# Performance work log

Hardware: AMD Instinct MI355X
Metric: run time of the kernel (lower is better)

## Reference

```python
import jax, jax.numpy as jnp
import numpy as np

NUM_FEATURES = 256   # 2**8
BOND_DIM = 16
N_CORES = 8          # log2(NUM_FEATURES)
BATCH = 262144


def _mpo_cores(mpo_weights, n, bond_dim):
    # Slice the flat parameter vector into n cores of shape (l, r, 2, 2).
    shapes = [(1, bond_dim, 2, 2)] + [(bond_dim, bond_dim, 2, 2)] * (n - 2) + [(bond_dim, 1, 2, 2)]
    cores, off = [], 0
    for s in shapes:
        sz = int(np.prod(s))
        cores.append(mpo_weights[off:off + sz].reshape(s))
        off += sz
    return cores


def _contract_mpo(cores):
    # Sequentially contract the tensor-train cores into the full (2^n, 2^n) matrix.
    # T has axes (bond, I, J) where I/J accumulate the row/col physical bits
    # in order i1..in / j1..jn, matching the original einsum + reshape.
    T = cores[0][0]          # (r, 2, 2)
    dim = 2
    for A in cores[1:]:      # A: (l, r2, 2, 2)
        T = jnp.einsum('aIJ,abkm->bIkJm', T, A).reshape(A.shape[1], dim * 2, dim * 2)
        dim *= 2
    return T[0]              # (2^n, 2^n)


def setup_inputs() -> dict:
    key = jax.random.key(0)
    k1, k2, k3 = jax.random.split(key, 3)
    total = 2 * 4 * BOND_DIM + (N_CORES - 2) * 4 * BOND_DIM ** 2  # 6272
    return {
        'x': jax.random.normal(k1, (BATCH, NUM_FEATURES), dtype=jnp.float32),
        'mpo_weights': jax.random.normal(k2, (total,), dtype=jnp.float32) * 0.1,
        'dense_kernel': jax.random.normal(k3, (NUM_FEATURES, 1), dtype=jnp.float32) * 0.1,
        'dense_bias': jnp.zeros((1,), dtype=jnp.float32),
    }


def reference(x, mpo_weights, dense_kernel, dense_bias):
    W = _contract_mpo(_mpo_cores(mpo_weights, N_CORES, BOND_DIM))  # (256, 256)
    h = jnp.square(x @ W)                                          # (B, 256)
    return h @ dense_kernel + dense_bias                           # (B, 1)
```

## Files before the change

kernel.cpp:

```cpp
#include <hip/hip_runtime.h>
#include <hip/hip_bf16.h>

typedef _Float16 half8 __attribute__((ext_vector_type(8)));
typedef float    floatx4 __attribute__((ext_vector_type(4)));

#define WSCALE      4096.0f
#define WSCALE_INV  (1.0f/(4096.0f*4096.0f))

#define T1_OFF   0
#define U_OFF    4096
#define WF16_OFF 8192

__global__ __launch_bounds__(1024)
void mpo_prep1(const float* __restrict__ w, float* __restrict__ ws) {
    __shared__ float wL[3136];
    __shared__ float sL[4352];
    const int tid = threadIdx.x;

    if (blockIdx.x == 0) {
        for (int i = tid; i < 3136; i += 1024) wL[i] = w[i];
        __syncthreads();
        if (tid < 256) {
            int li = tid;
            int mm = li & 3, kk = (li >> 2) & 3, c = li >> 4;
            int k1 = kk >> 1, k2 = kk & 1, m1 = mm >> 1, m2 = mm & 1;
            float s = 0.f;
            for (int b = 0; b < 16; ++b)
                s += wL[(b * 2 + k1) * 2 + m1] * wL[64 + ((b * 16 + c) * 2 + k2) * 2 + m2];
            sL[li] = s;
        }
        for (int li = tid; li < 4096; li += 1024) {
            int mm = li & 3, kk = (li >> 2) & 3, ac = li >> 4;
            int c = ac & 15, a = ac >> 4;
            int k1 = kk >> 1, k2 = kk & 1, m1 = mm >> 1, m2 = mm & 1;
            float s = 0.f;
            for (int b = 0; b < 16; ++b)
                s += wL[1088 + ((a * 16 + b) * 2 + k1) * 2 + m1]
                   * wL[2112 + ((b * 16 + c) * 2 + k2) * 2 + m2];
            sL[256 + li] = s;
        }
        __syncthreads();
        for (int idx = tid; idx < 4096; idx += 1024) {
            int J4 = idx & 15; int t = idx >> 4; int I4 = t & 15; int b = t >> 4;
            int I = I4 >> 2, k = I4 & 3, J = J4 >> 2, m = J4 & 3;
            float s = 0.f;
            for (int a = 0; a < 16; ++a)
                s += sL[a * 16 + I * 4 + J] * sL[256 + ((a * 16 + b) * 4 + k) * 4 + m];
            ws[T1_OFF + idx] = s;
        }
    } else {
        for (int i = tid; i < 3136; i += 1024) wL[i] = w[3136 + i];
        __syncthreads();
        for (int li = tid; li < 4096; li += 1024) {
            int mm = li & 3, kk = (li >> 2) & 3, ac = li >> 4;
            int c = ac & 15, a = ac >> 4;
            int k1 = kk >> 1, k2 = kk & 1, m1 = mm >> 1, m2 = mm & 1;
            float s = 0.f;
            for (int b = 0; b < 16; ++b)
                s += wL[((a * 16 + b) * 2 + k1) * 2 + m1]
                   * wL[1024 + ((b * 16 + c) * 2 + k2) * 2 + m2];
            sL[li] = s;
        }
        if (tid < 256) {
            int li = tid;
            int mm = li & 3, kk = (li >> 2) & 3, a = li >> 4;
            int k1 = kk >> 1, k2 = kk & 1, m1 = mm >> 1, m2 = mm & 1;
            float s = 0.f;
            for (int b = 0; b < 16; ++b)
                s += wL[2048 + ((a * 16 + b) * 2 + k1) * 2 + m1]
                   * wL[3072 + (b * 2 + k2) * 2 + m2];
            sL[4096 + li] = s;
        }
        __syncthreads();
        for (int idx = tid; idx < 4096; idx += 1024) {
            int m2 = idx & 3, k2 = (idx >> 2) & 3, mc = (idx >> 4) & 3,
                kc = (idx >> 6) & 3, a = idx >> 8;
            float s = 0.f;
            for (int b = 0; b < 16; ++b)
                s += sL[((a * 16 + b) * 4 + kc) * 4 + mc] * sL[4096 + (b * 4 + k2) * 4 + m2];
            ws[U_OFF + idx] = s;
        }
    }
}

__global__ __launch_bounds__(256)
void mpo_prep2(const float* __restrict__ ws, _Float16* __restrict__ Wf) {
    int idx = blockIdx.x * blockDim.x + threadIdx.x;
    int J4 = idx & 255, I4 = idx >> 8;
    int I16 = I4 >> 4, kc = (I4 >> 2) & 3, k2 = I4 & 3;
    int J16 = J4 >> 4, mc = (J4 >> 2) & 3, m2 = J4 & 3;
    const float* T1 = ws + T1_OFF;
    const float* U  = ws + U_OFF + (((kc * 4 + mc) * 4 + k2) * 4 + m2);
    float s = 0.f;
#pragma unroll
    for (int a = 0; a < 16; ++a)
        s += T1[(a * 16 + I16) * 16 + J16] * U[a * 256];
    int n = J4 >> 4, lr = J4 & 15, kk = I4 >> 5, gg = (I4 >> 3) & 3, j = I4 & 7;
    Wf[(((n * 8 + kk) * 64) + gg * 16 + lr) * 8 + j] = (_Float16)(s * WSCALE);
}

__global__ __launch_bounds__(512, 2)
void mpo_main(const float* __restrict__ x, const _Float16* __restrict__ Wf,
              const float* __restrict__ dk, const float* __restrict__ bias,
              float* __restrict__ out) {
    extern __shared__ _Float16 Wl[];
    float* dkL = reinterpret_cast<float*>(Wl + 65536);

    const int tid  = threadIdx.x;
    const int lane = tid & 63;
    const int wave = tid >> 6;
    const int lrow = lane & 15;
    const int g    = lane >> 4;

    const long blockbase = (long)blockIdx.x * 1024;
    const float* xb0 = x + (blockbase + wave * 16 + lrow) * 256 + g * 8;

    half8 a[8];
    floatx4 lo[8], hi[8];

#define SB()    __builtin_amdgcn_sched_barrier(0)
#define XLD(i, xn) do { const float* p_ = (xn) + (i) * 32;                                  \
                     lo[i] = __builtin_nontemporal_load(reinterpret_cast<const floatx4*>(p_));     \
                     hi[i] = __builtin_nontemporal_load(reinterpret_cast<const floatx4*>(p_ + 4)); \
                   } while (0)
#define XLD_ALL(xn) do { XLD(0,xn); XLD(1,xn); XLD(2,xn); XLD(3,xn);           \
                         XLD(4,xn); XLD(5,xn); XLD(6,xn); XLD(7,xn); } while (0)
#define XCVT(i) do { half8 f_;                                                 \
                     f_[0] = (_Float16)lo[i][0]; f_[1] = (_Float16)lo[i][1];   \
                     f_[2] = (_Float16)lo[i][2]; f_[3] = (_Float16)lo[i][3];   \
                     f_[4] = (_Float16)hi[i][0]; f_[5] = (_Float16)hi[i][1];   \
                     f_[6] = (_Float16)hi[i][2]; f_[7] = (_Float16)hi[i][3];   \
                     a[i] = f_; } while (0)
#define XCVT_ALL() do { XCVT(0); XCVT(1); XCVT(2); XCVT(3);                    \
                        XCVT(4); XCVT(5); XCVT(6); XCVT(7); } while (0)

    XLD_ALL(xb0);
    SB();
    {
        const floatx4* src = reinterpret_cast<const floatx4*>(Wf);
        floatx4* dst = reinterpret_cast<floatx4*>(Wl);
#pragma unroll
        for (int i = 0; i < 16; ++i)
            dst[tid + i * 512] = src[tid + i * 512];
    }
    if (tid < 256) dkL[tid] = dk[tid];
    const float bs = bias[0];
    __syncthreads();

    XCVT_ALL();
    SB();

    const half8* Wv = reinterpret_cast<const half8*>(Wl);

#pragma unroll 1
    for (int p = 0; p < 8; ++p) {
        if (p < 7) {
            const float* xn = xb0 + (p + 1) * (128 * 256);
            XLD_ALL(xn);
        }
        SB();

        float rp[4] = {0, 0, 0, 0};
#pragma unroll 1
        for (int n = 0; n < 16; ++n) {
            const float kv = dkL[n * 16 + lrow];
            const half8* Wn = Wv + n * 512 + lane;
            floatx4 c0 = {0, 0, 0, 0};
#pragma unroll
            for (int kk = 0; kk < 8; ++kk)
                c0 = __builtin_amdgcn_mfma_f32_16x16x32_f16(a[kk], Wn[kk * 64], c0, 0, 0, 0);
#pragma unroll
            for (int r = 0; r < 4; ++r)
                rp[r] += c0[r] * c0[r] * kv;
        }

        if (p < 7) { XCVT_ALL(); }
        SB();

#pragma unroll
        for (int r = 0; r < 4; ++r) {
            float v = rp[r];
            v += __shfl_xor(v, 1);
            v += __shfl_xor(v, 2);
            v += __shfl_xor(v, 4);
            v += __shfl_xor(v, 8);
            rp[r] = v;
        }
        if (lrow == 0) {
            floatx4 o;
#pragma unroll
            for (int r = 0; r < 4; ++r) o[r] = rp[r] * WSCALE_INV + bs;
            *reinterpret_cast<floatx4*>(out + blockbase + p * 128 + wave * 16 + g * 4) = o;
        }
    }
}

extern "C" void kernel_launch(void* const* d_in, const int* in_sizes, int n_in,
                              void* d_out, int out_size, void* d_ws, size_t ws_size,
                              hipStream_t stream) {
    const float* x    = (const float*)d_in[0];
    const float* w    = (const float*)d_in[1];
    const float* dk   = (const float*)d_in[2];
    const float* bias = (const float*)d_in[3];
    float* out = (float*)d_out;
    float* ws  = (float*)d_ws;

    _Float16* Wf16 = (_Float16*)(ws + WF16_OFF);

    static bool attr_set = false;
    if (!attr_set) {
        hipFuncSetAttribute((const void*)mpo_main,
                            hipFuncAttributeMaxDynamicSharedMemorySize, 132096);
        attr_set = true;
    }

    mpo_prep1<<<2, 1024, 0, stream>>>(w, ws);
    mpo_prep2<<<256, 256, 0, stream>>>(ws, Wf16);

    mpo_main<<<256, 512, 132096, stream>>>(x, Wf16, dk, bias, out);
}
```

Baseline: 70.41 us.

## Double-buffer x prefetch two tiles ahead and register-tile MPO prep contractions

The main kernel now keeps two register buffers for x (even/odd tiles), so each tile's loads are issued two iterations ahead and have a full MFMA pass to arrive before conversion. The prep kernel is rewritten to use 256 threads, each computing a 4x4 register tile with vectorized shared-memory reads and a vectorized weight load. Together these aim to hide global load latency in the main loop and shorten the serial prep stage. The extra 32 float4 registers for the second x buffer raise register pressure under the 2-blocks-per-CU launch bound and could cause spilling.

```diff
diff --git a/kernel.cpp b/kernel.cpp
--- a/kernel.cpp
+++ b/kernel.cpp
@@ -11,74 +11,127 @@
 #define U_OFF    4096
 #define WF16_OFF 8192
 
-__global__ __launch_bounds__(1024)
+__global__ __launch_bounds__(256)
 void mpo_prep1(const float* __restrict__ w, float* __restrict__ ws) {
-    __shared__ float wL[3136];
-    __shared__ float sL[4352];
+    __shared__ __align__(16) float wL[3136];
+    __shared__ __align__(16) float sL[4352];
     const int tid = threadIdx.x;
 
+    {
+        const floatx4* s4 = reinterpret_cast<const floatx4*>(w + blockIdx.x * 3136);
+        floatx4* d4 = reinterpret_cast<floatx4*>(wL);
+        for (int i = tid; i < 784; i += 256) d4[i] = s4[i];
+    }
+    __syncthreads();
+
     if (blockIdx.x == 0) {
-        for (int i = tid; i < 3136; i += 1024) wL[i] = w[i];
-        __syncthreads();
-        if (tid < 256) {
+        {
             int li = tid;
             int mm = li & 3, kk = (li >> 2) & 3, c = li >> 4;
             int k1 = kk >> 1, k2 = kk & 1, m1 = mm >> 1, m2 = mm & 1;
             float s = 0.f;
+#pragma unroll
             for (int b = 0; b < 16; ++b)
-                s += wL[(b * 2 + k1) * 2 + m1] * wL[64 + ((b * 16 + c) * 2 + k2) * 2 + m2];
+                s += wL[b * 4 + k1 * 2 + m1] * wL[64 + b * 64 + c * 4 + k2 * 2 + m2];
             sL[li] = s;
         }
-        for (int li = tid; li < 4096; li += 1024) {
-            int mm = li & 3, kk = (li >> 2) & 3, ac = li >> 4;
-            int c = ac & 15, a = ac >> 4;
-            int k1 = kk >> 1, k2 = kk & 1, m1 = mm >> 1, m2 = mm & 1;
-            float s = 0.f;
-            for (int b = 0; b < 16; ++b)
-                s += wL[1088 + ((a * 16 + b) * 2 + k1) * 2 + m1]
-                   * wL[2112 + ((b * 16 + c) * 2 + k2) * 2 + m2];
-            sL[256 + li] = s;
+        {
+            const int i0 = (tid >> 4) * 4, j0 = (tid & 15) * 4;
+            const float* Ab = wL + 1088 + (i0 >> 2) * 64;
+            const float* Bb = wL + 2112 + j0;
+            float acc[4][4] = {};
+#pragma unroll
+            for (int b = 0; b < 16; ++b) {
+                floatx4 ar = *reinterpret_cast<const floatx4*>(Ab + b * 4);
+                floatx4 br = *reinterpret_cast<const floatx4*>(Bb + b * 64);
+#pragma unroll
+                for (int r = 0; r < 4; ++r)
+#pragma unroll
+                    for (int s = 0; s < 4; ++s) acc[r][s] += ar[r] * br[s];
+            }
+#pragma unroll
+            for (int r = 0; r < 4; ++r)
+#pragma unroll
+            for (int s = 0; s < 4; ++s) {
+                int i = i0 + r, j = j0 + s;
+                sL[256 + (i >> 2) * 256 + (j >> 2) * 16 +
+                   ((i >> 1) & 1) * 8 + ((j >> 1) & 1) * 4 + (i & 1) * 2 + (j & 1)] = acc[r][s];
+            }
         }
         __syncthreads();
-        for (int idx = tid; idx < 4096; idx += 1024) {
-            int J4 = idx & 15; int t = idx >> 4; int I4 = t & 15; int b = t >> 4;
-            int I = I4 >> 2, k = I4 & 3, J = J4 >> 2, m = J4 & 3;
-            float s = 0.f;
-            for (int a = 0; a < 16; ++a)
-                s += sL[a * 16 + I * 4 + J] * sL[256 + ((a * 16 + b) * 4 + k) * 4 + m];
-            ws[T1_OFF + idx] = s;
+        {
+            const int p0 = (tid >> 6) * 4, q0 = (tid & 63) * 4;
+            float acc[4][4] = {};
+#pragma unroll
+            for (int a = 0; a < 16; ++a) {
+                floatx4 pr = *reinterpret_cast<const floatx4*>(sL + a * 16 + p0);
+                floatx4 qr = *reinterpret_cast<const floatx4*>(sL + 256 + a * 256 + q0);
+#pragma unroll
+                for (int r = 0; r < 4; ++r)
+#pragma unroll
+                    for (int s = 0; s < 4; ++s) acc[r][s] += pr[r] * qr[s];
+            }
+#pragma unroll
+            for (int r = 0; r < 4; ++r)
+#pragma unroll
+            for (int s = 0; s < 4; ++s) {
+                int p = p0 + r, q = q0 + s;
+                ws[T1_OFF + (q >> 4) * 256 + ((p >> 2) * 4 + ((q >> 2) & 3)) * 16 +
+                   (p & 3) * 4 + (q & 3)] = acc[r][s];
+            }
         }
     } else {
-        for (int i = tid; i < 3136; i += 1024) wL[i] = w[3136 + i];
-        __syncthreads();
-        for (int li = tid; li < 4096; li += 1024) {
-            int mm = li & 3, kk = (li >> 2) & 3, ac = li >> 4;
-            int c = ac & 15, a = ac >> 4;
-            int k1 = kk >> 1, k2 = kk & 1, m1 = mm >> 1, m2 = mm & 1;
-            float s = 0.f;
-            for (int b = 0; b < 16; ++b)
-                s += wL[((a * 16 + b) * 2 + k1) * 2 + m1]
-                   * wL[1024 + ((b * 16 + c) * 2 + k2) * 2 + m2];
-            sL[li] = s;
-        }
-        if (tid < 256) {
+        {
+            const int i0 = (tid >> 4) * 4, j0 = (tid & 15) * 4;
+            const float* Ab = wL + (i0 >> 2) * 64;
+            const float* Bb = wL + 1024 + j0;
+            float acc[4][4] = {};
+#pragma unroll
+            for (int b = 0; b < 16; ++b) {
+                floatx4 ar = *reinterpret_cast<const floatx4*>(Ab + b * 4);
+                floatx4 br = *reinterpret_cast<const floatx4*>(Bb + b * 64);
+#pragma unroll
+                for (int r = 0; r < 4; ++r)
+#pragma unroll
+                    for (int s = 0; s < 4; ++s) acc[r][s] += ar[r] * br[s];
+            }
+#pragma unroll
+            for (int r = 0; r < 4; ++r)
+#pragma unroll
+            for (int s = 0; s < 4; ++s) {
+                int i = i0 + r, j = j0 + s;
+                sL[(i >> 2) * 256 + (j >> 2) * 16 +
+                   ((i >> 1) & 1) * 8 + ((j >> 1) & 1) * 4 + (i & 1) * 2 + (j & 1)] = acc[r][s];
+            }
+        }
+        {
             int li = tid;
             int mm = li & 3, kk = (li >> 2) & 3, a = li >> 4;
             int k1 = kk >> 1, k2 = kk & 1, m1 = mm >> 1, m2 = mm & 1;
             float s = 0.f;
+#pragma unroll
             for (int b = 0; b < 16; ++b)
-                s += wL[2048 + ((a * 16 + b) * 2 + k1) * 2 + m1]
-                   * wL[3072 + (b * 2 + k2) * 2 + m2];
+                s += wL[2048 + a * 64 + b * 4 + k1 * 2 + m1] * wL[3072 + b * 4 + k2 * 2 + m2];
             sL[4096 + li] = s;
         }
         __syncthreads();
-        for (int idx = tid; idx < 4096; idx += 1024) {
-            int m2 = idx & 3, k2 = (idx >> 2) & 3, mc = (idx >> 4) & 3,
-                kc = (idx >> 6) & 3, a = idx >> 8;
-            float s = 0.f;
-            for (int b = 0; b < 16; ++b)
-                s += sL[((a * 16 + b) * 4 + kc) * 4 + mc] * sL[4096 + (b * 4 + k2) * 4 + m2];
-            ws[U_OFF + idx] = s;
+        {
+            const int r0 = (tid >> 2) * 4, q0 = (tid & 3) * 4;
+            float acc[4][4] = {};
+#pragma unroll
+            for (int b = 0; b < 16; ++b) {
+                floatx4 ar = *reinterpret_cast<const floatx4*>(sL + (r0 >> 4) * 256 + b * 16 + (r0 & 15));
+                floatx4 br = *reinterpret_cast<const floatx4*>(sL + 4096 + b * 16 + q0);
+#pragma unroll
+                for (int r = 0; r < 4; ++r)
+#pragma unroll
+                    for (int s = 0; s < 4; ++s) acc[r][s] += ar[r] * br[s];
+            }
+#pragma unroll
+            for (int r = 0; r < 4; ++r)
+#pragma unroll
+            for (int s = 0; s < 4; ++s)
+                ws[U_OFF + (r0 + r) * 16 + q0 + s] = acc[r][s];
         }
     }
 }
@@ -116,25 +169,62 @@
     const float* xb0 = x + (blockbase + wave * 16 + lrow) * 256 + g * 8;
 
     half8 a[8];
-    floatx4 lo[8], hi[8];
-
-#define SB()    __builtin_amdgcn_sched_barrier(0)
-#define XLD(i, xn) do { const float* p_ = (xn) + (i) * 32;                                  \
-                     lo[i] = __builtin_nontemporal_load(reinterpret_cast<const floatx4*>(p_));     \
-                     hi[i] = __builtin_nontemporal_load(reinterpret_cast<const floatx4*>(p_ + 4)); \
-                   } while (0)
-#define XLD_ALL(xn) do { XLD(0,xn); XLD(1,xn); XLD(2,xn); XLD(3,xn);           \
-                         XLD(4,xn); XLD(5,xn); XLD(6,xn); XLD(7,xn); } while (0)
-#define XCVT(i) do { half8 f_;                                                 \
-                     f_[0] = (_Float16)lo[i][0]; f_[1] = (_Float16)lo[i][1];   \
-                     f_[2] = (_Float16)lo[i][2]; f_[3] = (_Float16)lo[i][3];   \
-                     f_[4] = (_Float16)hi[i][0]; f_[5] = (_Float16)hi[i][1];   \
-                     f_[6] = (_Float16)hi[i][2]; f_[7] = (_Float16)hi[i][3];   \
+    floatx4 loE[8], hiE[8], loO[8], hiO[8];
+
+#define SB()  __builtin_amdgcn_sched_barrier(0)
+#define NTL(p) __builtin_nontemporal_load(reinterpret_cast<const floatx4*>(p))
+#define XLDE(i, xn) do { const float* p_ = (xn) + (i) * 32; loE[i] = NTL(p_); hiE[i] = NTL(p_ + 4); } while (0)
+#define XLDO(i, xn) do { const float* p_ = (xn) + (i) * 32; loO[i] = NTL(p_); hiO[i] = NTL(p_ + 4); } while (0)
+#define XLDE_ALL(xn) do { XLDE(0,xn); XLDE(1,xn); XLDE(2,xn); XLDE(3,xn); \
+                          XLDE(4,xn); XLDE(5,xn); XLDE(6,xn); XLDE(7,xn); } while (0)
+#define XLDO_ALL(xn) do { XLDO(0,xn); XLDO(1,xn); XLDO(2,xn); XLDO(3,xn); \
+                          XLDO(4,xn); XLDO(5,xn); XLDO(6,xn); XLDO(7,xn); } while (0)
+#define XCVTE(i) do { half8 f_;                                                \
+                     f_[0] = (_Float16)loE[i][0]; f_[1] = (_Float16)loE[i][1]; \
+                     f_[2] = (_Float16)loE[i][2]; f_[3] = (_Float16)loE[i][3]; \
+                     f_[4] = (_Float16)hiE[i][0]; f_[5] = (_Float16)hiE[i][1]; \
+                     f_[6] = (_Float16)hiE[i][2]; f_[7] = (_Float16)hiE[i][3]; \
                      a[i] = f_; } while (0)
-#define XCVT_ALL() do { XCVT(0); XCVT(1); XCVT(2); XCVT(3);                    \
-                        XCVT(4); XCVT(5); XCVT(6); XCVT(7); } while (0)
-
-    XLD_ALL(xb0);
+#define XCVTO(i) do { half8 f_;                                                \
+                     f_[0] = (_Float16)loO[i][0]; f_[1] = (_Float16)loO[i][1]; \
+                     f_[2] = (_Float16)loO[i][2]; f_[3] = (_Float16)loO[i][3]; \
+                     f_[4] = (_Float16)hiO[i][0]; f_[5] = (_Float16)hiO[i][1]; \
+                     f_[6] = (_Float16)hiO[i][2]; f_[7] = (_Float16)hiO[i][3]; \
+                     a[i] = f_; } while (0)
+#define XCVTE_ALL() do { XCVTE(0); XCVTE(1); XCVTE(2); XCVTE(3); \
+                         XCVTE(4); XCVTE(5); XCVTE(6); XCVTE(7); } while (0)
+#define XCVTO_ALL() do { XCVTO(0); XCVTO(1); XCVTO(2); XCVTO(3); \
+                         XCVTO(4); XCVTO(5); XCVTO(6); XCVTO(7); } while (0)
+
+#define NLOOP(rp) do {                                                           \
+    _Pragma("unroll 1")                                                          \
+    for (int n = 0; n < 16; ++n) {                                               \
+        const float kv = dkL[n * 16 + lrow];                                     \
+        const half8* Wn = Wv + n * 512 + lane;                                   \
+        floatx4 c0 = {0, 0, 0, 0};                                               \
+        _Pragma("unroll")                                                        \
+        for (int kk = 0; kk < 8; ++kk)                                           \
+            c0 = __builtin_amdgcn_mfma_f32_16x16x32_f16(a[kk], Wn[kk * 64], c0, 0, 0, 0); \
+        _Pragma("unroll")                                                        \
+        for (int r = 0; r < 4; ++r) rp[r] += c0[r] * c0[r] * kv;                 \
+    } } while (0)
+
+#define REDUCE_STORE(rp, p) do {                                                 \
+    _Pragma("unroll")                                                            \
+    for (int r = 0; r < 4; ++r) {                                                \
+        float v = rp[r];                                                         \
+        v += __shfl_xor(v, 1); v += __shfl_xor(v, 2);                            \
+        v += __shfl_xor(v, 4); v += __shfl_xor(v, 8);                            \
+        rp[r] = v;                                                               \
+    }                                                                            \
+    if (lrow == 0) {                                                             \
+        floatx4 o;                                                               \
+        _Pragma("unroll")                                                        \
+        for (int r = 0; r < 4; ++r) o[r] = rp[r] * WSCALE_INV + bs;              \
+        *reinterpret_cast<floatx4*>(out + blockbase + (p) * 128 + wave * 16 + g * 4) = o; \
+    } } while (0)
+
+    XLDE_ALL(xb0);
     SB();
     {
         const floatx4* src = reinterpret_cast<const floatx4*>(Wf);
@@ -146,51 +236,32 @@
     if (tid < 256) dkL[tid] = dk[tid];
     const float bs = bias[0];
     __syncthreads();
-
-    XCVT_ALL();
+    XLDO_ALL(xb0 + 128 * 256);
     SB();
+    XCVTE_ALL();
+    SB();
 
     const half8* Wv = reinterpret_cast<const half8*>(Wl);
 
 #pragma unroll 1
-    for (int p = 0; p < 8; ++p) {
-        if (p < 7) {
-            const float* xn = xb0 + (p + 1) * (128 * 256);
-            XLD_ALL(xn);
-        }
-        SB();
-
-        float rp[4] = {0, 0, 0, 0};
-#pragma unroll 1
-        for (int n = 0; n < 16; ++n) {
-            const float kv = dkL[n * 16 + lrow];
-            const half8* Wn = Wv + n * 512 + lane;
-            floatx4 c0 = {0, 0, 0, 0};
-#pragma unroll
-            for (int kk = 0; kk < 8; ++kk)
-                c0 = __builtin_amdgcn_mfma_f32_16x16x32_f16(a[kk], Wn[kk * 64], c0, 0, 0, 0);
-#pragma unroll
-            for (int r = 0; r < 4; ++r)
-                rp[r] += c0[r] * c0[r] * kv;
-        }
-
-        if (p < 7) { XCVT_ALL(); }
-        SB();
-
-#pragma unroll
-        for (int r = 0; r < 4; ++r) {
-            float v = rp[r];
-            v += __shfl_xor(v, 1);
-            v += __shfl_xor(v, 2);
-            v += __shfl_xor(v, 4);
-            v += __shfl_xor(v, 8);
-            rp[r] = v;
-        }
-        if (lrow == 0) {
-            floatx4 o;
-#pragma unroll
-            for (int r = 0; r < 4; ++r) o[r] = rp[r] * WSCALE_INV + bs;
-            *reinterpret_cast<floatx4*>(out + blockbase + p * 128 + wave * 16 + g * 4) = o;
+    for (int pp = 0; pp < 8; pp += 2) {
+        {
+            float rp[4] = {0, 0, 0, 0};
+            NLOOP(rp);
+            if (pp + 2 < 8) { XLDE_ALL(xb0 + (pp + 2) * (128 * 256)); }
+            SB();
+            REDUCE_STORE(rp, pp);
+            XCVTO_ALL();
+            SB();
+        }
+        {
+            float rp[4] = {0, 0, 0, 0};
+            NLOOP(rp);
+            if (pp + 3 < 8) { XLDO_ALL(xb0 + (pp + 3) * (128 * 256)); }
+            SB();
+            REDUCE_STORE(rp, pp + 1);
+            if (pp + 2 < 8) { XCVTE_ALL(); }
+            SB();
         }
     }
 }
@@ -214,7 +285,7 @@
         attr_set = true;
     }
 
-    mpo_prep1<<<2, 1024, 0, stream>>>(w, ws);
+    mpo_prep1<<<2, 256, 0, stream>>>(w, ws);
     mpo_prep2<<<256, 256, 0, stream>>>(ws, Wf16);
 
     mpo_main<<<256, 512, 132096, stream>>>(x, Wf16, dk, bias, out);
```

Measured after the change: 73.96 us. +5.0%, slower.
